# Kernel optimization log

Hardware: AMD Instinct MI355X
Metric: run time of the kernel (lower is better)

Reference implementation:

```python
import jax, jax.numpy as jnp
import numpy as np
from jax import lax

B, T, D, H, S = 256, 512, 256, 512, 8


def setup_inputs() -> dict:
    key = jax.random.key(0)
    ks = jax.random.split(key, 8)
    bound = 1.0 / np.sqrt(H)  # torch LSTMCell/Linear default init scale
    u = lambda k_, shp: jax.random.uniform(k_, shp, jnp.float32, -bound, bound)
    _input = jax.random.normal(ks[0], (B, T, D), jnp.float32)
    h0 = jax.random.normal(ks[1], (B, H), jnp.float32)
    c0 = jax.random.normal(ks[2], (B, H), jnp.float32)
    W_ih = u(ks[3], (4 * H, D))
    W_hh = u(ks[4], (4 * H, H))
    b_ih = u(ks[5], (4 * H,))
    b_hh = u(ks[6], (4 * H,))
    W_lin = u(ks[7], (D, H))
    b_lin = jnp.zeros((D,), jnp.float32)
    # random skip weights per module logic: w1~Bern; w2=1 if w1==0 else Bern; first S steps (1,0)
    rng = np.random.default_rng(0)
    w1 = rng.integers(0, 2, T)
    w2 = np.where(w1 == 0, 1, rng.integers(0, 2, T))
    w1[:S] = 1
    w2[:S] = 0
    return {
        "_input": _input, "h0": h0, "c0": c0,
        "W_ih": W_ih, "W_hh": W_hh, "b_ih": b_ih, "b_hh": b_hh,
        "W_lin": W_lin, "b_lin": b_lin,
        "w1": jnp.asarray(w1, jnp.int32), "w2": jnp.asarray(w2, jnp.int32),
        "time_steps": T, "skip_size": S,
    }


def _lstm_cell(x, h, c, W_ih, W_hh, b_ih, b_hh):
    gates = x @ W_ih.T + b_ih + h @ W_hh.T + b_hh  # [B, 4H]
    i, f, g, o = jnp.split(gates, 4, axis=-1)
    i, f, o = jax.nn.sigmoid(i), jax.nn.sigmoid(f), jax.nn.sigmoid(o)
    c_new = f * c + i * jnp.tanh(g)
    h_new = o * jnp.tanh(c_new)
    return h_new, c_new


def reference(_input, h0, c0, W_ih, W_hh, b_ih, b_hh, W_lin, b_lin, w1, w2, time_steps, skip_size):
    # decoder-mode RSCN: feed previous linear(h) as next input
    buf_h = jnp.repeat(h0[None], skip_size, axis=0)  # FIFO queue as ring buffer [S,B,H]
    buf_c = jnp.repeat(c0[None], skip_size, axis=0)

    def step(carry, xs):
        h_feed, h, c, bh, bc = carry
        w1t, w2t, t = xs
        h_new, c_new = _lstm_cell(h_feed, h, c, W_ih, W_hh, b_ih, b_hh)
        pos = t % skip_size
        skip_h, skip_c = bh[pos], bc[pos]  # queue.get() (oldest)
        bh = bh.at[pos].set(h_new)          # queue.put(new)
        bc = bc.at[pos].set(c_new)
        a = w1t.astype(h_new.dtype)
        b = w2t.astype(h_new.dtype)
        norm = 1.0 / (a + b)
        comb_h = (a * h_new + b * jnp.tanh(skip_h)) * norm
        comb_c = (a * c_new + b * jnp.tanh(skip_c)) * norm
        out = comb_h @ W_lin.T + b_lin  # [B, D]
        return (out, comb_h, comb_c, bh, bc), out

    xs = (w1[:time_steps], w2[:time_steps], jnp.arange(time_steps))
    carry0 = (_input[:, 0, :], h0, c0, buf_h, buf_c)
    (_, h_fin, c_fin, _, _), outs = lax.scan(step, carry0, xs)
    return outs.transpose(1, 0, 2), h_fin, c_fin  # [B,T,D], final (h, c)
```

## Files before the change

### kernel.cpp

```cpp
#include <hip/hip_runtime.h>
#include <math.h>

#define BB 256
#define TT 512
#define DD 256
#define HH 512
#define SS 8
#define G4H 2048
#define BH (BB*HH)
#define OUT_BASE ((size_t)BB*TT*DD)
#define NGRP 16
#define GR 16
#define XSLOT_U32 4096
#define FSTRIDE 16

typedef _Float16 f16;
typedef __attribute__((ext_vector_type(8))) _Float16 f16x8;
typedef __attribute__((ext_vector_type(4))) float    f32x4;

__device__ __forceinline__ float sigm(float x) { return 1.f / (1.f + __expf(-x)); }
__device__ __forceinline__ float ftanh(float x) {
  x = fminf(15.f, fmaxf(-15.f, x));
  float e = __expf(-2.f * x);
  return (1.f - e) / (1.f + e);
}


__global__ __launch_bounds__(256) void prep_wbig16(
    const float* __restrict__ W_ih, const float* __restrict__ W_hh,
    const float* __restrict__ W_lin, f16* __restrict__ Wbig16)
{
  __shared__ float As[64][20];
  __shared__ float Bs[16][68];
  const int n0 = blockIdx.x * 64;
  const int j0 = blockIdx.y * 64;
  const int tid = threadIdx.x;
  const int tn = tid >> 4, tj = tid & 15;
  float acc[4][4] = {};
  for (int k0 = 0; k0 < DD; k0 += 16) {
    { int r = tid >> 2, c = (tid & 3) * 4;
      *(float4*)&As[r][c] = *(const float4*)&W_ih[(size_t)(n0 + r) * DD + k0 + c]; }
    { int r = tid >> 4, c = (tid & 15) * 4;
      *(float4*)&Bs[r][c] = *(const float4*)&W_lin[(size_t)(k0 + r) * HH + j0 + c]; }
    __syncthreads();
    #pragma unroll
    for (int k = 0; k < 16; ++k) {
      float a[4], bv[4];
      #pragma unroll
      for (int i = 0; i < 4; ++i) a[i] = As[tn*4+i][k];
      #pragma unroll
      for (int m = 0; m < 4; ++m) bv[m] = Bs[k][tj*4+m];
      #pragma unroll
      for (int i = 0; i < 4; ++i)
        #pragma unroll
        for (int m = 0; m < 4; ++m)
          acc[i][m] = fmaf(a[i], bv[m], acc[i][m]);
    }
    __syncthreads();
  }
  #pragma unroll
  for (int i = 0; i < 4; ++i) {
    int n = n0 + tn*4 + i;
    #pragma unroll
    for (int m = 0; m < 4; ++m) {
      int j = j0 + tj*4 + m;
      Wbig16[(size_t)n*HH + j] = (f16)(acc[i][m] + W_hh[(size_t)n*HH + j]);
    }
  }
}

__global__ void prep_bias(const float* __restrict__ b_ih, const float* __restrict__ b_hh,
                          const float* __restrict__ W_ih, const float* __restrict__ b_lin,
                          float* __restrict__ bias0, float* __restrict__ bias1)
{
  int n = blockIdx.x * 256 + threadIdx.x;
  float s = b_ih[n] + b_hh[n];
  float d = 0.f;
  for (int k = 0; k < DD; ++k) d = fmaf(W_ih[(size_t)n*DD + k], b_lin[k], d);
  bias0[n] = s;
  bias1[n] = s + d;
}

#define NIH (G4H*DD)
#define NHH (G4H*HH)
__global__ void prep_cvtw(const float* __restrict__ W_ih, const float* __restrict__ W_hh,
                          const float* __restrict__ W_lin,
                          f16* __restrict__ Wih16, f16* __restrict__ Whh16,
                          f16* __restrict__ Wlin16)
{
  int e = blockIdx.x * 256 + threadIdx.x;
  if (e < NIH) Wih16[e] = (f16)W_ih[e];
  else if (e < NIH + NHH) Whh16[e - NIH] = (f16)W_hh[e - NIH];
  else Wlin16[e - NIH - NHH] = (f16)W_lin[e - NIH - NHH];
}

__global__ void prep_init(const float* __restrict__ x0, const float* __restrict__ h0,
                          const float* __restrict__ c0,
                          const int* __restrict__ w1, const int* __restrict__ w2,
                          float* __restrict__ bh, float* __restrict__ bc,
                          f16* __restrict__ x0hi, f16* __restrict__ x0lo,
                          f16* __restrict__ h0hi, f16* __restrict__ h0lo,
                          float4* __restrict__ stepc,
                          int* __restrict__ flags)
{
  int e = blockIdx.x * 256 + threadIdx.x;
  int r = e & (BH - 1);
  bh[e] = h0[r];
  bc[e] = c0[r];
  if (e < BH) {
    float v = h0[e];
    f16 hi = (f16)v;
    h0hi[e] = hi;
    h0lo[e] = (f16)(v - (float)hi);
  }
  if (e < BB*DD) {
    int b = e >> 8, d = e & 255;
    float v = x0[(size_t)b*(TT*DD) + d];
    f16 hi = (f16)v;
    x0hi[e] = hi;
    x0lo[e] = (f16)(v - (float)hi);
  }
  if (e < TT) {
    float a1 = (float)w1[e], a2 = (float)w2[e];
    stepc[e] = make_float4(a1, a2, 1.f / (a1 + a2), 0.f);
  }
  if (e < 4096) flags[e] = 0;
}


__device__ __forceinline__ void stage_stripe(const unsigned* __restrict__ Xs,
                                             int w, f16* lds, int lane) {
  #pragma unroll
  for (int i = 0; i < 2; ++i) {
    int q = i * 64 + lane;
    int row = q >> 3, u = q & 7;
    const char* src = (const char*)Xs + w * 2048 + row * 128 +
                      ((u ^ (row & 7)) << 4);
    __builtin_amdgcn_global_load_lds(
        (const __attribute__((address_space(1))) void*)src,
        (__attribute__((address_space(3))) void*)((char*)lds + w * 2048 + i * 1024),
        16, 0, 0x11 );
  }
}

__device__ __forceinline__ void gemm16(const f16x8 (&wA)[16], const f16x8 (&wB)[16],
                                       const f16* lds, int lane,
                                       f32x4& acc0, f32x4& acc1) {
  const int r  = lane & 15;
  const int kc = lane >> 4;
  #pragma unroll
  for (int ks = 0; ks < 16; ++ks) {
    int role_k = ks >> 1;
    int u = ((ks & 1) << 2) + kc;
    int off = role_k * 2048 + r * 128 + ((u ^ (r & 7)) << 4);
    f16x8 a = *(const f16x8*)((const char*)lds + off);
    acc0 = __builtin_amdgcn_mfma_f32_16x16x32_f16(a, wA[ks], acc0, 0, 0, 0);
    acc1 = __builtin_amdgcn_mfma_f32_16x16x32_f16(a, wB[ks], acc1, 0, 0, 0);
  }
}

__global__ __launch_bounds__(512, 2) void lstm_persist(
    const f16* __restrict__ x0hi, const f16* __restrict__ x0lo,
    const f16* __restrict__ h0hi, const f16* __restrict__ h0lo,
    const float* __restrict__ c0,
    const f16* __restrict__ Wih16, const f16* __restrict__ Whh16,
    const f16* __restrict__ Wbig16, const f16* __restrict__ Wlin16,
    const float* __restrict__ bias0, const float* __restrict__ bias1,
    const float* __restrict__ b_lin,
    const float4* __restrict__ stepc,
    unsigned* __restrict__ X,
    float* __restrict__ bh, float* __restrict__ bc,
    int* __restrict__ flags,
    float* __restrict__ outp)
{
  __shared__ f16 LdsA[8192];
  __shared__ float gbuf[4096];

  const int tid  = threadIdx.x;
  const int lane = tid & 63;
  const int wv   = tid >> 6;
  const int bid  = blockIdx.x;
  const bool isG = bid < 128;
  const int grp  = isG ? (bid & 15) : (bid - 128);
  const int role = bid >> 4;
  const int b0   = grp * GR;
  const int r16  = lane & 15;
  const int kc   = lane >> 4;
  const int ksel = kc * 8;

  int* gflag = flags + grp * 9 * FSTRIDE;

  int rowA, rowB;
  const f16* wsrc;
  if (isG) {
    rowA = (wv & 3) * 512 + role * 64 + (wv >> 2) * 32 + r16;
    rowB = rowA + 16;
    wsrc = Wbig16;
  } else {
    rowA = wv * 32 + r16;
    rowB = rowA + 16;
    wsrc = Wlin16;
  }
  f16x8 wA[16], wB[16];
  #pragma unroll
  for (int ks = 0; ks < 16; ++ks) {
    wA[ks] = *(const f16x8*)(wsrc + (size_t)rowA * HH + ks * 32 + ksel);
    wB[ks] = *(const f16x8*)(wsrc + (size_t)rowB * HH + ks * 32 + ksel);
  }

  if (isG) {
    int   eidx[2];
    float creg[2];
    const int jl = tid & 63;
    const int jg = role * 64 + jl;
    const float bI = bias1[jg],        bF = bias1[512 + jg];
    const float bG = bias1[1024 + jg], bO = bias1[1536 + jg];
    #pragma unroll
    for (int i = 0; i < 2; ++i) {
      int c = i * 512 + tid;
      int bl = c >> 6;
      eidx[i] = (b0 + bl) * HH + jg;
      creg[i] = c0[eidx[i]];
    }

    for (int t = 0; t < TT; ++t) {
      const float4 sc = stepc[t];
      const int pos = t & (SS - 1);
      float shv[2], scv[2];
      #pragma unroll
      for (int i = 0; i < 2; ++i) {
        int bx = pos * BH + eidx[i];
        shv[i] = bh[bx];
        scv[i] = bc[bx];
      }

      if (t > 0) {
        if (lane == 0) {
          while (__hip_atomic_load(&gflag[wv * FSTRIDE], __ATOMIC_RELAXED,
                                   __HIP_MEMORY_SCOPE_AGENT) < t) {}
        } else if (wv == 0 && lane == 1 && t >= 4) {
          while (__hip_atomic_load(&gflag[8 * FSTRIDE], __ATOMIC_RELAXED,
                                   __HIP_MEMORY_SCOPE_AGENT) < t - 3) {}
        }
        stage_stripe(X + (size_t)(((t - 1) & 3) * NGRP + grp) * XSLOT_U32,
                     wv, LdsA, lane);
      }

      f32x4 acc0, acc1;
      #pragma unroll
      for (int i = 0; i < 4; ++i) { acc0[i] = 0.f; acc1[i] = 0.f; }
      if (t == 0) {
        const f16* arh = x0hi + (size_t)(b0 + r16) * DD;
        const f16* arl = x0lo + (size_t)(b0 + r16) * DD;
        const f16* wap = Wih16 + (size_t)rowA * DD;
        const f16* wbp = Wih16 + (size_t)rowB * DD;
        #pragma unroll
        for (int ks = 0; ks < 8; ++ks) {
          int ko = ks * 32 + ksel;
          f16x8 wa = *(const f16x8*)(wap + ko);
          f16x8 wb = *(const f16x8*)(wbp + ko);
          f16x8 ah = *(const f16x8*)(arh + ko);
          f16x8 al = *(const f16x8*)(arl + ko);
          acc0 = __builtin_amdgcn_mfma_f32_16x16x32_f16(ah, wa, acc0, 0, 0, 0);
          acc1 = __builtin_amdgcn_mfma_f32_16x16x32_f16(ah, wb, acc1, 0, 0, 0);
          acc0 = __builtin_amdgcn_mfma_f32_16x16x32_f16(al, wa, acc0, 0, 0, 0);
          acc1 = __builtin_amdgcn_mfma_f32_16x16x32_f16(al, wb, acc1, 0, 0, 0);
        }
        const f16* brh = h0hi + (size_t)(b0 + r16) * HH;
        const f16* brl = h0lo + (size_t)(b0 + r16) * HH;
        const f16* qap = Whh16 + (size_t)rowA * HH;
        const f16* qbp = Whh16 + (size_t)rowB * HH;
        #pragma unroll
        for (int ks = 0; ks < 16; ++ks) {
          int ko = ks * 32 + ksel;
          f16x8 wa = *(const f16x8*)(qap + ko);
          f16x8 wb = *(const f16x8*)(qbp + ko);
          f16x8 ah = *(const f16x8*)(brh + ko);
          f16x8 al = *(const f16x8*)(brl + ko);
          acc0 = __builtin_amdgcn_mfma_f32_16x16x32_f16(ah, wa, acc0, 0, 0, 0);
          acc1 = __builtin_amdgcn_mfma_f32_16x16x32_f16(ah, wb, acc1, 0, 0, 0);
          acc0 = __builtin_amdgcn_mfma_f32_16x16x32_f16(al, wa, acc0, 0, 0, 0);
          acc1 = __builtin_amdgcn_mfma_f32_16x16x32_f16(al, wb, acc1, 0, 0, 0);
        }
        __syncthreads();
      } else {
        __syncthreads();
        gemm16(wA, wB, LdsA, lane, acc0, acc1);
      }

      {
        const int g4 = wv & 3, jh = wv >> 2;
        #pragma unroll
        for (int rg = 0; rg < 4; ++rg) {
          int m  = kc * 4 + rg;
          int j0 = jh * 32 + r16;
          int cs0 = (j0      + 16 * kc) & 63;
          int cs1 = (j0 + 16 + 16 * kc) & 63;
          gbuf[g4 * 1024 + m * 64 + cs0] = acc0[rg];
          gbuf[g4 * 1024 + m * 64 + cs1] = acc1[rg];
        }
      }
      __syncthreads();

      const float a1 = sc.x, a2 = sc.y, nrm = sc.z;
      float baI = bI, baF = bF, baG = bG, baO = bO;
      if (t == 0) {
        baI = bias0[jg];        baF = bias0[512 + jg];
        baG = bias0[1024 + jg]; baO = bias0[1536 + jg];
      }
      unsigned* Xw = X + (size_t)((t & 3) * NGRP + grp) * XSLOT_U32;
      float hnv[2], cnv[2], chv[2];
      #pragma unroll
      for (int i = 0; i < 2; ++i) {
        int c = i * 512 + tid;
        int bl = c >> 6;
        int jj = c & 63;
        int gofs = bl * 64 + ((jj + 16 * (bl >> 2)) & 63);
        float pi = gbuf[gofs]        + baI;
        float pf = gbuf[1024 + gofs] + baF;
        float pg = gbuf[2048 + gofs] + baG;
        float po = gbuf[3072 + gofs] + baO;
        float i_ = sigm(pi), f_ = sigm(pf), o_ = sigm(po), g_ = ftanh(pg);
        float cnew = fmaf(f_, creg[i], i_ * g_);
        float hnew = o_ * ftanh(cnew);
        float ch = (a1 * hnew + a2 * ftanh(shv[i])) * nrm;
        hnv[i] = hnew; cnv[i] = cnew; chv[i] = ch;
        f16 hv = (f16)ch;
        unsigned hb = (unsigned)*(const unsigned short*)&hv;
        unsigned part = (unsigned)__shfl_xor((int)hb, 1);
        if ((tid & 1) == 0)
          __hip_atomic_store(&Xw[role * 512 + bl * 32 + (jl >> 1)], hb | (part << 16),
                             __ATOMIC_RELAXED, __HIP_MEMORY_SCOPE_AGENT);
      }
      __syncthreads();
      if (tid == 0)
        __hip_atomic_store(&gflag[role * FSTRIDE], t + 1, __ATOMIC_RELAXED,
                           __HIP_MEMORY_SCOPE_AGENT);

      #pragma unroll
      for (int i = 0; i < 2; ++i) {
        float cc = (a1 * cnv[i] + a2 * ftanh(scv[i])) * nrm;
        creg[i] = cc;
        int bx = pos * BH + eidx[i];
        bh[bx] = hnv[i];
        bc[bx] = cnv[i];
        if (t == TT - 1) {
          __builtin_nontemporal_store(chv[i], &outp[OUT_BASE + eidx[i]]);
          __builtin_nontemporal_store(cc,     &outp[OUT_BASE + BH + eidx[i]]);
        }
      }
    }
  } else {
    const float bld0 = b_lin[rowA];
    const float bld1 = b_lin[rowB];
    for (int s = 0; s < TT; ++s) {
      if (lane == 0) {
        while (__hip_atomic_load(&gflag[wv * FSTRIDE], __ATOMIC_RELAXED,
                                 __HIP_MEMORY_SCOPE_AGENT) < s + 1) {}
      }
      stage_stripe(X + (size_t)((s & 3) * NGRP + grp) * XSLOT_U32, wv, LdsA, lane);
      __syncthreads();
      if (tid == 0)
        __hip_atomic_store(&gflag[8 * FSTRIDE], s + 1, __ATOMIC_RELAXED,
                           __HIP_MEMORY_SCOPE_AGENT);
      f32x4 acc0, acc1;
      #pragma unroll
      for (int i = 0; i < 4; ++i) { acc0[i] = 0.f; acc1[i] = 0.f; }
      gemm16(wA, wB, LdsA, lane, acc0, acc1);
      const size_t tbase = (size_t)s * DD + wv * 32 + r16;
      #pragma unroll
      for (int rg = 0; rg < 4; ++rg) {
        int m = kc * 4 + rg;
        __builtin_nontemporal_store(acc0[rg] + bld0,
                                    &outp[(size_t)(b0 + m) * (TT*DD) + tbase]);
        __builtin_nontemporal_store(acc1[rg] + bld1,
                                    &outp[(size_t)(b0 + m) * (TT*DD) + tbase + 16]);
      }
      __syncthreads();
    }
  }
}


extern "C" void kernel_launch(void* const* d_in, const int* in_sizes, int n_in,
                              void* d_out, int out_size, void* d_ws, size_t ws_size,
                              hipStream_t stream)
{
  const float* x0    = (const float*)d_in[0];
  const float* h0    = (const float*)d_in[1];
  const float* c0    = (const float*)d_in[2];
  const float* W_ih  = (const float*)d_in[3];
  const float* W_hh  = (const float*)d_in[4];
  const float* b_ih  = (const float*)d_in[5];
  const float* b_hh  = (const float*)d_in[6];
  const float* W_lin = (const float*)d_in[7];
  const float* b_lin = (const float*)d_in[8];
  const int*   w1    = (const int*)d_in[9];
  const int*   w2    = (const int*)d_in[10];

  char* p = (char*)d_ws;
  f16* Wbig16 = (f16*)p;            p += (size_t)G4H*HH*2;
  f16* Wih16  = (f16*)p;            p += (size_t)G4H*DD*2;
  f16* Whh16  = (f16*)p;            p += (size_t)G4H*HH*2;
  f16* Wlin16 = (f16*)p;            p += (size_t)DD*HH*2;
  f16* x0hi   = (f16*)p;            p += (size_t)BB*DD*2;
  f16* x0lo   = (f16*)p;            p += (size_t)BB*DD*2;
  f16* h0hi   = (f16*)p;            p += (size_t)BH*2;
  f16* h0lo   = (f16*)p;            p += (size_t)BH*2;
  unsigned* X = (unsigned*)p;       p += (size_t)4*NGRP*XSLOT_U32*4;
  float* bh   = (float*)p;          p += (size_t)SS*BH*4;
  float* bc   = (float*)p;          p += (size_t)SS*BH*4;
  float* bias0= (float*)p;          p += G4H*4;
  float* bias1= (float*)p;          p += G4H*4;
  float4* stepc = (float4*)p;       p += (size_t)TT*16;
  int*  flags = (int*)p;            p += 4096*4;
  float* outp = (float*)d_out;

  hipLaunchKernelGGL(prep_wbig16, dim3(32, 8), dim3(256), 0, stream,
                     W_ih, W_hh, W_lin, Wbig16);
  hipLaunchKernelGGL(prep_bias, dim3(8), dim3(256), 0, stream,
                     b_ih, b_hh, W_ih, b_lin, bias0, bias1);
  hipLaunchKernelGGL(prep_cvtw, dim3(6656), dim3(256), 0, stream,
                     W_ih, W_hh, W_lin, Wih16, Whh16, Wlin16);
  hipLaunchKernelGGL(prep_init, dim3(4096), dim3(256), 0, stream,
                     x0, h0, c0, w1, w2, bh, bc, x0hi, x0lo, h0hi, h0lo, stepc, flags);

  hipLaunchKernelGGL(lstm_persist, dim3(128 + NGRP), dim3(512), 0, stream,
                     x0hi, x0lo, h0hi, h0lo, c0, Wih16, Whh16, Wbig16, Wlin16,
                     bias0, bias1, b_lin, stepc, X, bh, bc, flags, outp);
}
```

Measured before the change: 1.425 ms.

## Halve block size so each wave computes all four gates in registers, dropping LDS gate exchange

The persistent LSTM kernel now runs 256-thread blocks. Each wave holds weight rows for all four gates (i,f,g,o) of its 16 hidden units, so the cell update reads MFMA accumulators directly instead of scattering them through a shared gbuf and synchronising twice. Each wave now stages two stripes and polls two producer flags. The cost is twice the weight registers per thread (64 f16x8 vectors) and fewer waves per block, which may hurt latency hiding or spill registers.

```diff
diff --git a/kernel.cpp b/kernel.cpp
--- a/kernel.cpp
+++ b/kernel.cpp
@@ -143,9 +143,8 @@
   }
 }
 
-__device__ __forceinline__ void gemm16(const f16x8 (&wA)[16], const f16x8 (&wB)[16],
-                                       const f16* lds, int lane,
-                                       f32x4& acc0, f32x4& acc1) {
+__device__ __forceinline__ void gemm4(const f16x8 (&w)[4][16], const f16* lds,
+                                      int lane, f32x4 (&acc)[4]) {
   const int r  = lane & 15;
   const int kc = lane >> 4;
   #pragma unroll
@@ -154,12 +153,13 @@
     int u = ((ks & 1) << 2) + kc;
     int off = role_k * 2048 + r * 128 + ((u ^ (r & 7)) << 4);
     f16x8 a = *(const f16x8*)((const char*)lds + off);
-    acc0 = __builtin_amdgcn_mfma_f32_16x16x32_f16(a, wA[ks], acc0, 0, 0, 0);
-    acc1 = __builtin_amdgcn_mfma_f32_16x16x32_f16(a, wB[ks], acc1, 0, 0, 0);
-  }
-}
-
-__global__ __launch_bounds__(512, 2) void lstm_persist(
+    #pragma unroll
+    for (int g = 0; g < 4; ++g)
+      acc[g] = __builtin_amdgcn_mfma_f32_16x16x32_f16(a, w[g][ks], acc[g], 0, 0, 0);
+  }
+}
+
+__global__ __launch_bounds__(256, 1) void lstm_persist(
     const f16* __restrict__ x0hi, const f16* __restrict__ x0lo,
     const f16* __restrict__ h0hi, const f16* __restrict__ h0lo,
     const float* __restrict__ c0,
@@ -174,7 +174,6 @@
     float* __restrict__ outp)
 {
   __shared__ f16 LdsA[8192];
-  __shared__ float gbuf[4096];
 
   const int tid  = threadIdx.x;
   const int lane = tid & 63;
@@ -190,117 +189,99 @@
 
   int* gflag = flags + grp * 9 * FSTRIDE;
 
-  int rowA, rowB;
+  int rowG[4];
   const f16* wsrc;
   if (isG) {
-    rowA = (wv & 3) * 512 + role * 64 + (wv >> 2) * 32 + r16;
-    rowB = rowA + 16;
+    #pragma unroll
+    for (int g = 0; g < 4; ++g) rowG[g] = g * 512 + role * 64 + wv * 16 + r16;
     wsrc = Wbig16;
   } else {
-    rowA = wv * 32 + r16;
-    rowB = rowA + 16;
+    #pragma unroll
+    for (int g = 0; g < 4; ++g) rowG[g] = wv * 64 + g * 16 + r16;
     wsrc = Wlin16;
   }
-  f16x8 wA[16], wB[16];
+  f16x8 wreg[4][16];
   #pragma unroll
-  for (int ks = 0; ks < 16; ++ks) {
-    wA[ks] = *(const f16x8*)(wsrc + (size_t)rowA * HH + ks * 32 + ksel);
-    wB[ks] = *(const f16x8*)(wsrc + (size_t)rowB * HH + ks * 32 + ksel);
-  }
+  for (int g = 0; g < 4; ++g)
+    #pragma unroll
+    for (int ks = 0; ks < 16; ++ks)
+      wreg[g][ks] = *(const f16x8*)(wsrc + (size_t)rowG[g] * HH + ks * 32 + ksel);
 
   if (isG) {
-    int   eidx[2];
-    float creg[2];
-    const int jl = tid & 63;
-    const int jg = role * 64 + jl;
+    const int jg = role * 64 + wv * 16 + r16;
+    const int jl = wv * 16 + r16;
     const float bI = bias1[jg],        bF = bias1[512 + jg];
     const float bG = bias1[1024 + jg], bO = bias1[1536 + jg];
-    #pragma unroll
-    for (int i = 0; i < 2; ++i) {
-      int c = i * 512 + tid;
-      int bl = c >> 6;
-      eidx[i] = (b0 + bl) * HH + jg;
-      creg[i] = c0[eidx[i]];
+    int   eidx[4];
+    float creg[4];
+    #pragma unroll
+    for (int rg = 0; rg < 4; ++rg) {
+      eidx[rg] = (b0 + kc * 4 + rg) * HH + jg;
+      creg[rg] = c0[eidx[rg]];
     }
 
     for (int t = 0; t < TT; ++t) {
       const float4 sc = stepc[t];
       const int pos = t & (SS - 1);
-      float shv[2], scv[2];
-      #pragma unroll
-      for (int i = 0; i < 2; ++i) {
-        int bx = pos * BH + eidx[i];
-        shv[i] = bh[bx];
-        scv[i] = bc[bx];
+      float shv[4], scv[4];
+      #pragma unroll
+      for (int rg = 0; rg < 4; ++rg) {
+        int bx = pos * BH + eidx[rg];
+        shv[rg] = bh[bx];
+        scv[rg] = bc[bx];
       }
 
       if (t > 0) {
-        if (lane == 0) {
-          while (__hip_atomic_load(&gflag[wv * FSTRIDE], __ATOMIC_RELAXED,
-                                   __HIP_MEMORY_SCOPE_AGENT) < t) {}
-        } else if (wv == 0 && lane == 1 && t >= 4) {
-          while (__hip_atomic_load(&gflag[8 * FSTRIDE], __ATOMIC_RELAXED,
-                                   __HIP_MEMORY_SCOPE_AGENT) < t - 3) {}
+        int fidx = -1, target = t;
+        if (lane < 2) fidx = (2 * wv + lane) * FSTRIDE;
+        else if (wv == 0 && lane == 2 && t >= 4) { fidx = 8 * FSTRIDE; target = t - 3; }
+        if (fidx >= 0) {
+          while (__hip_atomic_load(&gflag[fidx], __ATOMIC_RELAXED,
+                                   __HIP_MEMORY_SCOPE_AGENT) < target) {}
         }
-        stage_stripe(X + (size_t)(((t - 1) & 3) * NGRP + grp) * XSLOT_U32,
-                     wv, LdsA, lane);
-      }
-
-      f32x4 acc0, acc1;
-      #pragma unroll
-      for (int i = 0; i < 4; ++i) { acc0[i] = 0.f; acc1[i] = 0.f; }
+        const unsigned* Xs = X + (size_t)(((t - 1) & 3) * NGRP + grp) * XSLOT_U32;
+        stage_stripe(Xs, 2 * wv,     LdsA, lane);
+        stage_stripe(Xs, 2 * wv + 1, LdsA, lane);
+      }
+      __syncthreads();
+
+      f32x4 acc[4];
+      #pragma unroll
+      for (int g = 0; g < 4; ++g)
+        #pragma unroll
+        for (int i = 0; i < 4; ++i) acc[g][i] = 0.f;
       if (t == 0) {
         const f16* arh = x0hi + (size_t)(b0 + r16) * DD;
         const f16* arl = x0lo + (size_t)(b0 + r16) * DD;
-        const f16* wap = Wih16 + (size_t)rowA * DD;
-        const f16* wbp = Wih16 + (size_t)rowB * DD;
         #pragma unroll
         for (int ks = 0; ks < 8; ++ks) {
           int ko = ks * 32 + ksel;
-          f16x8 wa = *(const f16x8*)(wap + ko);
-          f16x8 wb = *(const f16x8*)(wbp + ko);
           f16x8 ah = *(const f16x8*)(arh + ko);
           f16x8 al = *(const f16x8*)(arl + ko);
-          acc0 = __builtin_amdgcn_mfma_f32_16x16x32_f16(ah, wa, acc0, 0, 0, 0);
-          acc1 = __builtin_amdgcn_mfma_f32_16x16x32_f16(ah, wb, acc1, 0, 0, 0);
-          acc0 = __builtin_amdgcn_mfma_f32_16x16x32_f16(al, wa, acc0, 0, 0, 0);
-          acc1 = __builtin_amdgcn_mfma_f32_16x16x32_f16(al, wb, acc1, 0, 0, 0);
+          #pragma unroll
+          for (int g = 0; g < 4; ++g) {
+            f16x8 w = *(const f16x8*)(Wih16 + (size_t)rowG[g] * DD + ko);
+            acc[g] = __builtin_amdgcn_mfma_f32_16x16x32_f16(ah, w, acc[g], 0, 0, 0);
+            acc[g] = __builtin_amdgcn_mfma_f32_16x16x32_f16(al, w, acc[g], 0, 0, 0);
+          }
         }
         const f16* brh = h0hi + (size_t)(b0 + r16) * HH;
         const f16* brl = h0lo + (size_t)(b0 + r16) * HH;
-        const f16* qap = Whh16 + (size_t)rowA * HH;
-        const f16* qbp = Whh16 + (size_t)rowB * HH;
         #pragma unroll
         for (int ks = 0; ks < 16; ++ks) {
           int ko = ks * 32 + ksel;
-          f16x8 wa = *(const f16x8*)(qap + ko);
-          f16x8 wb = *(const f16x8*)(qbp + ko);
           f16x8 ah = *(const f16x8*)(brh + ko);
           f16x8 al = *(const f16x8*)(brl + ko);
-          acc0 = __builtin_amdgcn_mfma_f32_16x16x32_f16(ah, wa, acc0, 0, 0, 0);
-          acc1 = __builtin_amdgcn_mfma_f32_16x16x32_f16(ah, wb, acc1, 0, 0, 0);
-          acc0 = __builtin_amdgcn_mfma_f32_16x16x32_f16(al, wa, acc0, 0, 0, 0);
-          acc1 = __builtin_amdgcn_mfma_f32_16x16x32_f16(al, wb, acc1, 0, 0, 0);
+          #pragma unroll
+          for (int g = 0; g < 4; ++g) {
+            f16x8 w = *(const f16x8*)(Whh16 + (size_t)rowG[g] * HH + ko);
+            acc[g] = __builtin_amdgcn_mfma_f32_16x16x32_f16(ah, w, acc[g], 0, 0, 0);
+            acc[g] = __builtin_amdgcn_mfma_f32_16x16x32_f16(al, w, acc[g], 0, 0, 0);
+          }
         }
-        __syncthreads();
       } else {
-        __syncthreads();
-        gemm16(wA, wB, LdsA, lane, acc0, acc1);
-      }
-
-      {
-        const int g4 = wv & 3, jh = wv >> 2;
-        #pragma unroll
-        for (int rg = 0; rg < 4; ++rg) {
-          int m  = kc * 4 + rg;
-          int j0 = jh * 32 + r16;
-          int cs0 = (j0      + 16 * kc) & 63;
-          int cs1 = (j0 + 16 + 16 * kc) & 63;
-          gbuf[g4 * 1024 + m * 64 + cs0] = acc0[rg];
-          gbuf[g4 * 1024 + m * 64 + cs1] = acc1[rg];
-        }
-      }
-      __syncthreads();
+        gemm4(wreg, LdsA, lane, acc);
+      }
 
       const float a1 = sc.x, a2 = sc.y, nrm = sc.z;
       float baI = bI, baF = bF, baG = bG, baO = bO;
@@ -309,27 +290,24 @@
         baG = bias0[1024 + jg]; baO = bias0[1536 + jg];
       }
       unsigned* Xw = X + (size_t)((t & 3) * NGRP + grp) * XSLOT_U32;
-      float hnv[2], cnv[2], chv[2];
-      #pragma unroll
-      for (int i = 0; i < 2; ++i) {
-        int c = i * 512 + tid;
-        int bl = c >> 6;
-        int jj = c & 63;
-        int gofs = bl * 64 + ((jj + 16 * (bl >> 2)) & 63);
-        float pi = gbuf[gofs]        + baI;
-        float pf = gbuf[1024 + gofs] + baF;
-        float pg = gbuf[2048 + gofs] + baG;
-        float po = gbuf[3072 + gofs] + baO;
+      float hnv[4], cnv[4], chv[4];
+      #pragma unroll
+      for (int rg = 0; rg < 4; ++rg) {
+        float pi = acc[0][rg] + baI;
+        float pf = acc[1][rg] + baF;
+        float pg = acc[2][rg] + baG;
+        float po = acc[3][rg] + baO;
         float i_ = sigm(pi), f_ = sigm(pf), o_ = sigm(po), g_ = ftanh(pg);
-        float cnew = fmaf(f_, creg[i], i_ * g_);
+        float cnew = fmaf(f_, creg[rg], i_ * g_);
         float hnew = o_ * ftanh(cnew);
-        float ch = (a1 * hnew + a2 * ftanh(shv[i])) * nrm;
-        hnv[i] = hnew; cnv[i] = cnew; chv[i] = ch;
+        float ch = (a1 * hnew + a2 * ftanh(shv[rg])) * nrm;
+        hnv[rg] = hnew; cnv[rg] = cnew; chv[rg] = ch;
         f16 hv = (f16)ch;
         unsigned hb = (unsigned)*(const unsigned short*)&hv;
         unsigned part = (unsigned)__shfl_xor((int)hb, 1);
-        if ((tid & 1) == 0)
-          __hip_atomic_store(&Xw[role * 512 + bl * 32 + (jl >> 1)], hb | (part << 16),
+        if ((r16 & 1) == 0)
+          __hip_atomic_store(&Xw[role * 512 + (kc * 4 + rg) * 32 + (jl >> 1)],
+                             hb | (part << 16),
                              __ATOMIC_RELAXED, __HIP_MEMORY_SCOPE_AGENT);
       }
       __syncthreads();
@@ -338,44 +316,48 @@
                            __HIP_MEMORY_SCOPE_AGENT);
 
       #pragma unroll
-      for (int i = 0; i < 2; ++i) {
-        float cc = (a1 * cnv[i] + a2 * ftanh(scv[i])) * nrm;
-        creg[i] = cc;
-        int bx = pos * BH + eidx[i];
-        bh[bx] = hnv[i];
-        bc[bx] = cnv[i];
+      for (int rg = 0; rg < 4; ++rg) {
+        float cc = (a1 * cnv[rg] + a2 * ftanh(scv[rg])) * nrm;
+        creg[rg] = cc;
+        int bx = pos * BH + eidx[rg];
+        bh[bx] = hnv[rg];
+        bc[bx] = cnv[rg];
         if (t == TT - 1) {
-          __builtin_nontemporal_store(chv[i], &outp[OUT_BASE + eidx[i]]);
-          __builtin_nontemporal_store(cc,     &outp[OUT_BASE + BH + eidx[i]]);
+          __builtin_nontemporal_store(chv[rg], &outp[OUT_BASE + eidx[rg]]);
+          __builtin_nontemporal_store(cc,      &outp[OUT_BASE + BH + eidx[rg]]);
         }
       }
     }
   } else {
-    const float bld0 = b_lin[rowA];
-    const float bld1 = b_lin[rowB];
+    float bld[4];
+    #pragma unroll
+    for (int g = 0; g < 4; ++g) bld[g] = b_lin[rowG[g]];
     for (int s = 0; s < TT; ++s) {
-      if (lane == 0) {
-        while (__hip_atomic_load(&gflag[wv * FSTRIDE], __ATOMIC_RELAXED,
+      if (lane < 2) {
+        int fidx = (2 * wv + lane) * FSTRIDE;
+        while (__hip_atomic_load(&gflag[fidx], __ATOMIC_RELAXED,
                                  __HIP_MEMORY_SCOPE_AGENT) < s + 1) {}
       }
-      stage_stripe(X + (size_t)((s & 3) * NGRP + grp) * XSLOT_U32, wv, LdsA, lane);
+      const unsigned* Xs = X + (size_t)((s & 3) * NGRP + grp) * XSLOT_U32;
+      stage_stripe(Xs, 2 * wv,     LdsA, lane);
+      stage_stripe(Xs, 2 * wv + 1, LdsA, lane);
       __syncthreads();
       if (tid == 0)
         __hip_atomic_store(&gflag[8 * FSTRIDE], s + 1, __ATOMIC_RELAXED,
                            __HIP_MEMORY_SCOPE_AGENT);
-      f32x4 acc0, acc1;
-      #pragma unroll
-      for (int i = 0; i < 4; ++i) { acc0[i] = 0.f; acc1[i] = 0.f; }
-      gemm16(wA, wB, LdsA, lane, acc0, acc1);
-      const size_t tbase = (size_t)s * DD + wv * 32 + r16;
-      #pragma unroll
-      for (int rg = 0; rg < 4; ++rg) {
-        int m = kc * 4 + rg;
-        __builtin_nontemporal_store(acc0[rg] + bld0,
-                                    &outp[(size_t)(b0 + m) * (TT*DD) + tbase]);
-        __builtin_nontemporal_store(acc1[rg] + bld1,
-                                    &outp[(size_t)(b0 + m) * (TT*DD) + tbase + 16]);
-      }
+      f32x4 acc[4];
+      #pragma unroll
+      for (int g = 0; g < 4; ++g)
+        #pragma unroll
+        for (int i = 0; i < 4; ++i) acc[g][i] = 0.f;
+      gemm4(wreg, LdsA, lane, acc);
+      const size_t srow = (size_t)s * DD;
+      #pragma unroll
+      for (int g = 0; g < 4; ++g)
+        #pragma unroll
+        for (int rg = 0; rg < 4; ++rg)
+          __builtin_nontemporal_store(acc[g][rg] + bld[g],
+              &outp[(size_t)(b0 + kc * 4 + rg) * (TT*DD) + srow + rowG[g]]);
       __syncthreads();
     }
   }
@@ -425,7 +407,7 @@
   hipLaunchKernelGGL(prep_init, dim3(4096), dim3(256), 0, stream,
                      x0, h0, c0, w1, w2, bh, bc, x0hi, x0lo, h0hi, h0lo, stepc, flags);
 
-  hipLaunchKernelGGL(lstm_persist, dim3(128 + NGRP), dim3(512), 0, stream,
+  hipLaunchKernelGGL(lstm_persist, dim3(128 + NGRP), dim3(256), 0, stream,
                      x0hi, x0lo, h0hi, h0lo, c0, Wih16, Whh16, Wbig16, Wlin16,
                      bias0, bias1, b_lin, stepc, X, bh, bc, flags, outp);
 }
```

After: 1.618 ms. 1.14x slower.
